# Optimization experiments

Measured on AMD Instinct MI355X. Metric: run time of the kernel, lower is better.

The kernel has to match this reference:

```python
import jax, jax.numpy as jnp
import numpy as np

T, NB, XD, HD, HC = 512, 30, 4096, 512, 32


def gru_cell(x, h, Wih, Whh, bih, bhh):
    # torch nn.GRU gate order: r, z, n
    gi = x @ Wih.T + bih  # [N, 3H]
    gh = h @ Whh.T + bhh
    i_r, i_z, i_n = jnp.split(gi, 3, axis=-1)
    h_r, h_z, h_n = jnp.split(gh, 3, axis=-1)
    r = jax.nn.sigmoid(i_r + h_r)
    z = jax.nn.sigmoid(i_z + h_z)
    n = jnp.tanh(i_n + r * h_n)
    return (1.0 - z) * n + z * h


def setup_inputs() -> dict:
    key = jax.random.key(0)
    ks = jax.random.split(key, 28)
    f32 = jnp.float32
    def rn(k, shape, s=0.05):
        return jax.random.normal(k, shape, dtype=f32) * s
    flow = jax.random.normal(ks[0], (1, T, NB + 1, XD), dtype=f32)
    x = jax.random.normal(ks[1], (1, T, 4), dtype=f32)
    # structured y: track id == bbox slot + 1 when present, 0 otherwise
    present = jax.random.uniform(ks[2], (T, NB)) > 0.3
    present = present.at[:, 0].set(True)
    tid = jnp.where(present, jnp.arange(1, NB + 1)[None, :], 0)
    x1 = jax.random.randint(ks[3], (T, NB), 1, 1080)
    y1 = jax.random.randint(ks[4], (T, NB), 1, 720)
    x2 = jax.random.randint(ks[5], (T, NB), 1, 1080)
    y2 = jax.random.randint(ks[6], (T, NB), 1, 720)
    lab = jax.random.randint(ks[7], (T, NB), 0, 2)
    y = jnp.stack([tid, x1, y1, x2, y2, lab], axis=-1).astype(jnp.int32)[None]
    return {
        'x': x, 'y': y, 'flow': flow,
        'W_phi': rn(ks[8], (XD, HD)), 'b_phi': rn(ks[9], (HD,)),
        'Wih0': rn(ks[10], (3 * HD, 2 * HD)), 'Whh0': rn(ks[11], (3 * HD, HD)),
        'bih0': rn(ks[12], (3 * HD,)), 'bhh0': rn(ks[13], (3 * HD,)),
        'Wih1': rn(ks[14], (3 * HD, HD)), 'Whh1': rn(ks[15], (3 * HD, HD)),
        'bih1': rn(ks[16], (3 * HD,)), 'bhh1': rn(ks[17], (3 * HD,)),
        'Wihc': rn(ks[18], (3 * HC, 4)), 'Whhc': rn(ks[19], (3 * HC, HC)),
        'bihc': rn(ks[20], (3 * HC,)), 'bhhc': rn(ks[21], (3 * HC,)),
        'W1': rn(ks[22], (HD + HC, 256)), 'b1': rn(ks[23], (256,)),
        'W2': rn(ks[24], (256, 2)), 'b2': rn(ks[25], (2,)),
        'wa': rn(ks[26], (HD,)), 'wac': rn(ks[27], (HC,)),
    }


def reference(x, y, flow, W_phi, b_phi, Wih0, Whh0, bih0, bhh0, Wih1, Whh1,
              bih1, bhh1, Wihc, Whhc, bihc, bhhc, W1, b1, W2, b2, wa, wac):
    dt = flow.dtype
    feats = flow[0]      # [T, 31, XD]
    yb_all = y[0]        # [T, 30, 6]
    norm = jnp.array([1080.0, 720.0, 1080.0, 720.0], dtype=dt)

    def att(hmat, w, present):
        # spatial attention: softmax over present tracks of tanh(h) @ w
        s = jnp.tanh(hmat) @ w                               # [30]
        smax = jnp.max(jnp.where(present, s, -1e30))
        e = jnp.where(present, jnp.exp(s - smax), 0.0)
        a = e / jnp.maximum(e.sum(), 1e-9)
        return hmat * a[:, None]

    def step(carry, inp):
        H0, H1, Hc, prev = carry
        feat, yb = inp
        xv = jax.nn.relu(feat @ W_phi + b_phi)               # [31, HD]
        img = jnp.broadcast_to(xv[0], (NB, HD))
        x_t = jnp.concatenate([xv[1:], img], axis=-1)        # [30, 2*HD]
        present = yb[:, 0] != 0
        keep = prev.astype(dt)[:, None]                      # state valid only if track seen last frame
        h0 = H0 * keep
        h1 = H1 * keep
        hc = Hc * keep
        cor = yb[:, 1:5].astype(dt) / norm                   # [30, 4]
        hc_n = gru_cell(cor, hc, Wihc, Whhc, bihc, bhhc)     # [30, HC]
        h0_n = gru_cell(x_t, h0, Wih0, Whh0, bih0, bhh0)     # [30, HD]
        h1_n = gru_cell(h0_n, h1, Wih1, Whh1, bih1, bhh1)    # [30, HD]
        o = jnp.concatenate([h1_n, hc_n], axis=-1)
        o = jax.nn.relu(o @ W1 + b1) @ W2 + b2               # [30, 2]
        logp = jax.nn.log_softmax(o, axis=-1)
        tgt = yb[:, 5].astype(jnp.int32)
        # weighted CE with mean reduction over a single sample == plain NLL
        nll = -jnp.take_along_axis(logp, tgt[:, None], axis=1)[:, 0]
        pm = present.astype(dt)
        loss = jnp.sum(nll * pm)
        H0a = att(h0_n, wa, present)
        H1a = att(h1_n, wa, present)
        Hca = att(hc_n, wac, present)
        return (H0a, H1a, Hca, present), (loss, o * pm[:, None])

    init = (jnp.zeros((NB, HD), dt), jnp.zeros((NB, HD), dt),
            jnp.zeros((NB, HC), dt), jnp.zeros((NB,), bool))
    _, (losses, outs) = jax.lax.scan(step, init, (feats, yb_all))
    return losses.sum(), outs
```

## Files before the change

### kernel.cpp

```cpp
#include <hip/hip_runtime.h>

#define TT   512
#define NBOX 30
#define HDIM 512
#define M1 (TT*31)
#define N1 HDIM
#define K1 4096
#define M2 (TT*NBOX)
#define N2 (3*HDIM)
#define K2 (2*HDIM)
#define NWG 256

#define DYN_FLOATS 40924
#define DYN_BYTES  (DYN_FLOATS * 4)

__device__ __forceinline__ float4 ld4(const float* p) { return *(const float4*)p; }
__device__ __forceinline__ float dot4(float4 a, float4 b) { return a.x*b.x + a.y*b.y + a.z*b.z + a.w*b.w; }
__device__ __forceinline__ float sigf(float x) { return 1.f / (1.f + __expf(-x)); }
__device__ __forceinline__ float thf(float x)  { return 1.f - 2.f / (1.f + __expf(2.f*x)); }

__device__ __forceinline__ float ldg_c(const float* p) {
    return __hip_atomic_load((float*)p, __ATOMIC_RELAXED, __HIP_MEMORY_SCOPE_AGENT);
}
__device__ __forceinline__ void stg_c(float* p, float v) {
    __hip_atomic_store(p, v, __ATOMIC_RELAXED, __HIP_MEMORY_SCOPE_AGENT);
}
__device__ __forceinline__ float2 ldg_c2(const float* p) {
    unsigned long long u = __hip_atomic_load((unsigned long long*)p, __ATOMIC_RELAXED, __HIP_MEMORY_SCOPE_AGENT);
    float2 r;
    r.x = __uint_as_float((unsigned)u);
    r.y = __uint_as_float((unsigned)(u >> 32));
    return r;
}
__device__ __forceinline__ void stg_c2(float* p, float a, float b) {
    unsigned long long u = ((unsigned long long)__float_as_uint(b) << 32) | (unsigned long long)__float_as_uint(a);
    __hip_atomic_store((unsigned long long*)p, u, __ATOMIC_RELAXED, __HIP_MEMORY_SCOPE_AGENT);
}

__global__ __launch_bounds__(256) void gemm_phi(const float* __restrict__ A,
                                                const float* __restrict__ B,
                                                const float* __restrict__ bias,
                                                float* __restrict__ C) {
    __shared__ float As[16][68];
    __shared__ float Bs[16][68];
    const int tid = threadIdx.x;
    const int m0 = blockIdx.x * 64;
    const int n0 = blockIdx.y * 64;
    const int am = tid >> 2, ak = (tid & 3) << 2;
    const int bk = tid >> 4, bn = (tid & 15) << 2;
    const int ty = tid >> 4, tx = tid & 15;
    float acc[4][4] = {};
    for (int k0 = 0; k0 < K1; k0 += 16) {
        const float4 av = *(const float4*)&A[(size_t)(m0 + am) * K1 + k0 + ak];
        const float4 bv = *(const float4*)&B[(size_t)(k0 + bk) * N1 + n0 + bn];
        __syncthreads();
        As[ak + 0][am] = av.x; As[ak + 1][am] = av.y; As[ak + 2][am] = av.z; As[ak + 3][am] = av.w;
        *(float4*)&Bs[bk][bn] = bv;
        __syncthreads();
#pragma unroll
        for (int kk = 0; kk < 16; ++kk) {
            const float4 a = *(const float4*)&As[kk][ty << 2];
            const float4 b = *(const float4*)&Bs[kk][tx << 2];
            const float ar[4] = {a.x, a.y, a.z, a.w};
            const float br[4] = {b.x, b.y, b.z, b.w};
#pragma unroll
            for (int i = 0; i < 4; ++i)
#pragma unroll
                for (int j = 0; j < 4; ++j) acc[i][j] = fmaf(ar[i], br[j], acc[i][j]);
        }
    }
    const float4 bsv = *(const float4*)&bias[n0 + (tx << 2)];
    const float bb[4] = {bsv.x, bsv.y, bsv.z, bsv.w};
#pragma unroll
    for (int i = 0; i < 4; ++i) {
        const int m = m0 + (ty << 2) + i;
        float4 o;
        o.x = fmaxf(acc[i][0] + bb[0], 0.f);
        o.y = fmaxf(acc[i][1] + bb[1], 0.f);
        o.z = fmaxf(acc[i][2] + bb[2], 0.f);
        o.w = fmaxf(acc[i][3] + bb[3], 0.f);
        *(float4*)&C[(size_t)m * N1 + n0 + (tx << 2)] = o;
    }
}

__global__ __launch_bounds__(256) void gemm_gi0(const float* __restrict__ xv,
                                                const float* __restrict__ Wih0,
                                                const float* __restrict__ bih0,
                                                float* __restrict__ C) {
    __shared__ float As[16][68];
    __shared__ float Bs[16][68];
    const int tid = threadIdx.x;
    const int m0 = blockIdx.x * 64;
    const int n0 = blockIdx.y * 64;
    const int am = tid >> 2, ak = (tid & 3) << 2;
    const int bn_ = tid >> 2, bkq = (tid & 3) << 2;
    const int ty = tid >> 4, tx = tid & 15;
    const int r = m0 + am;
    const int t = r / 30;
    const int j = r - t * 30;
    const float* rowTrk = xv + ((size_t)(t * 31 + 1 + j) << 9);
    const float* rowImg = xv + ((size_t)(t * 31) << 9);
    float acc[4][4] = {};
    for (int k0 = 0; k0 < K2; k0 += 16) {
        const int kg = k0 + ak;
        const float4 av = (kg < 512) ? *(const float4*)&rowTrk[kg]
                                     : *(const float4*)&rowImg[kg - 512];
        const float4 wv = *(const float4*)&Wih0[(size_t)(n0 + bn_) * K2 + k0 + bkq];
        __syncthreads();
        As[ak + 0][am] = av.x; As[ak + 1][am] = av.y; As[ak + 2][am] = av.z; As[ak + 3][am] = av.w;
        Bs[bkq + 0][bn_] = wv.x; Bs[bkq + 1][bn_] = wv.y; Bs[bkq + 2][bn_] = wv.z; Bs[bkq + 3][bn_] = wv.w;
        __syncthreads();
#pragma unroll
        for (int kk = 0; kk < 16; ++kk) {
            const float4 a = *(const float4*)&As[kk][ty << 2];
            const float4 b = *(const float4*)&Bs[kk][tx << 2];
            const float ar[4] = {a.x, a.y, a.z, a.w};
            const float br[4] = {b.x, b.y, b.z, b.w};
#pragma unroll
            for (int i = 0; i < 4; ++i)
#pragma unroll
                for (int jq = 0; jq < 4; ++jq) acc[i][jq] = fmaf(ar[i], br[jq], acc[i][jq]);
        }
    }
    const float4 bsv = *(const float4*)&bih0[n0 + (tx << 2)];
    const float bb[4] = {bsv.x, bsv.y, bsv.z, bsv.w};
#pragma unroll
    for (int i = 0; i < 4; ++i) {
        const int m = m0 + (ty << 2) + i;
        float4 o;
        o.x = acc[i][0] + bb[0];
        o.y = acc[i][1] + bb[1];
        o.z = acc[i][2] + bb[2];
        o.w = acc[i][3] + bb[3];
        *(float4*)&C[(size_t)m * N2 + n0 + (tx << 2)] = o;
    }
}

__global__ __launch_bounds__(256) void gic_kernel(const int* __restrict__ y,
                                                  const float* __restrict__ Wihc,
                                                  const float* __restrict__ bihc,
                                                  float* __restrict__ gic) {
    const int idx = blockIdx.x * 256 + threadIdx.x;
    if (idx >= M2 * 96) return;
    const int g = idx % 96;
    const int tj = idx / 96;
    const int* yb = y + (size_t)tj * 6;
    const float c0 = (float)yb[1] * (1.f / 1080.f);
    const float c1 = (float)yb[2] * (1.f / 720.f);
    const float c2 = (float)yb[3] * (1.f / 1080.f);
    const float c3 = (float)yb[4] * (1.f / 720.f);
    gic[idx] = bihc[g] + c0 * Wihc[g * 4 + 0] + c1 * Wihc[g * 4 + 1]
                       + c2 * Wihc[g * 4 + 2] + c3 * Wihc[g * 4 + 3];
}

__global__ void transpose_w1(const float* __restrict__ W1, float* __restrict__ W1T) {
    const int idx = blockIdx.x * 256 + threadIdx.x;
    if (idx >= 544 * 256) return;
    const int c = idx % 544, u = idx / 544;
    W1T[idx] = W1[c * 256 + u];
}

__global__ void init_k(unsigned* bar) {
    for (int i = threadIdx.x; i < 1088; i += 256) bar[i] = 0u;
}

__device__ __forceinline__ void gbar(unsigned* bar, unsigned ep, int w) {
    __syncthreads();
    if (threadIdx.x == 0) {
        asm volatile("" ::: "memory");
        const int g = w >> 4;
        unsigned* gcnt  = bar + g * 32;
        unsigned* gflag = bar + 544 + g * 32;
        const unsigned tgt = ep * 16u;
        unsigned prev = __hip_atomic_fetch_add(gcnt, 1u, __ATOMIC_RELAXED, __HIP_MEMORY_SCOPE_AGENT);
        if (prev + 1u == tgt) {
            unsigned prevr = __hip_atomic_fetch_add(bar + 512, 1u, __ATOMIC_RELAXED, __HIP_MEMORY_SCOPE_AGENT);
            if (prevr + 1u == tgt) {
                for (int i = 0; i < 16; ++i)
                    __hip_atomic_store(bar + 544 + i * 32, ep, __ATOMIC_RELAXED, __HIP_MEMORY_SCOPE_AGENT);
            } else {
                while (__hip_atomic_load(gflag, __ATOMIC_RELAXED, __HIP_MEMORY_SCOPE_AGENT) < ep)
                    __builtin_amdgcn_s_sleep(2);
            }
        } else {
            while (__hip_atomic_load(gflag, __ATOMIC_RELAXED, __HIP_MEMORY_SCOPE_AGENT) < ep)
                __builtin_amdgcn_s_sleep(2);
        }
        asm volatile("" ::: "memory");
    }
    __syncthreads();
}

__device__ __forceinline__ void softmax30_lane(int lane, float sj, int pres, float* outp) {
    float mv = pres ? sj : -1e30f;
    for (int off = 32; off; off >>= 1) mv = fmaxf(mv, __shfl_xor(mv, off));
    float ev = pres ? __expf(sj - mv) : 0.f;
    float sum = ev;
    for (int off = 32; off; off >>= 1) sum += __shfl_xor(sum, off);
    const float inv = 1.f / fmaxf(sum, 1e-9f);
    if (lane < NBOX) outp[lane] = ev * inv;
}

__device__ __forceinline__ void coord_gemv_elem(const float* chc, const float* Whhc, int e, float* cz) {
    const int j = e >> 5, c = e & 31;
    const float* hr = chc + j * 32;
#pragma unroll
    for (int m2 = 0; m2 < 3; ++m2) {
        const float* wr = Whhc + (size_t)(c + 32 * m2) * 32;
        float a = 0.f;
#pragma unroll
        for (int c2 = 0; c2 < 32; c2 += 4) a += dot4(ld4(hr + c2), ld4(wr + c2));
        cz[m2] = a;
    }
}

__device__ __forceinline__ void coord_comb_elem(float* chc, const float* gp, const float* bhhc,
                                                const float* csca, float* hcout, int e, const float* cz) {
    const int j = e >> 5, c = e & 31;
    const float s = csca[j];
    const float r = sigf(gp[j*96 + c]      + s*cz[0] + bhhc[c]);
    const float z = sigf(gp[j*96 + 32 + c] + s*cz[1] + bhhc[32+c]);
    const float n = thf (gp[j*96 + 64 + c] + r*(s*cz[2] + bhhc[64+c]));
    const float hn = (1.f - z)*n + z*(s*chc[e]);
    chc[e] = hn;
    stg_c(hcout + e, hn);
}

struct PArgs {
    const float *gi0, *gic;
    const float *Whh0, *Wih1, *Whh1, *Whhc;
    const float *bhh0, *bih1, *bhh1, *bhhc;
    const float *W1T, *b1, *W2, *b2, *wa, *wac;
    const int *y;
    float *h0g, *h1g, *hcg, *partials, *lossbuf, *out;
    unsigned *bar;
};

__global__ __launch_bounds__(256, 1) void persist(PArgs A) {
    extern __shared__ float smem[];
    float* Hs0  = smem;
    float* Hs1  = smem + 15480;
    float* Wp   = smem + 30960;
    float* gi_s = smem + 40248;
    float* Z0s  = smem + 40428;
    float* Z1s  = smem + 40608;
    float* sm0  = smem + 40788;
    float* sm1  = smem + 40820;
    float* redF = smem + 40852;

    const int w = blockIdx.x;
    const int tid = threadIdx.x;
    const bool isCoord = (w == NWG - 1);
    unsigned ep = 0;
    float lossSum = 0.f;

    if (!isCoord) {
#pragma unroll
        for (int i = 0; i < 9; ++i) {
            const int fid = tid + 256 * i;
            const int slot = fid >> 7;
            const int k4 = (fid & 127) << 2;
            const int sl = slot % 6;
            const int col = (sl % 3) * 512 + 2 * w + ((sl >= 3) ? 1 : 0);
            const float* mat = (slot < 6) ? A.Whh0 : (slot < 12) ? A.Wih1 : A.Whh1;
            *(float4*)&Wp[slot * 516 + k4] = ld4(mat + (size_t)col * 512 + k4);
        }
    } else {
        for (int i = tid; i < 1024; i += 256) Wp[i] = 0.f;
    }
    if (tid < 180) Z1s[tid] = 0.f;

    const int cjX = tid >> 1, ciX = tid & 1, cX = 2 * w + ciX;
    float b0r=0,b0z=0,b0n=0,b1r=0,b1z=0,b1n=0;
    if (tid < 60) {
        b0r = A.bhh0[cX]; b0z = A.bhh0[512+cX]; b0n = A.bhh0[1024+cX];
        b1r = A.bhh1[cX]; b1z = A.bhh1[512+cX]; b1n = A.bhh1[1024+cX];
    }
    float biA = 0.f, biB = 0.f;
    {
        const int q = tid & 7;
        if (tid < 240 && q >= 3 && q < 6) {
            const int slA = 2 * (q - 3), slB = slA + 1;
            biA = A.bih1[(slA % 3) * 512 + 2 * w + ((slA >= 3) ? 1 : 0)];
            biB = A.bih1[(slB % 3) * 512 + 2 * w + ((slB >= 3) ? 1 : 0)];
        }
    }
    float clb=0,c20=0,c21=0, clb2=0,c202=0,c212=0;
    if (!isCoord) { clb = A.b1[w]; c20 = A.W2[2*w]; c21 = A.W2[2*w+1]; }
    if (w == 254) { clb2 = A.b1[255]; c202 = A.W2[510]; c212 = A.W2[511]; }

    float cz0[3]={0,0,0}, cz1[3]={0,0,0}, cz2[3]={0,0,0}, cz3[3]={0,0,0};

    if (tid < 60) {
        const float* gp = A.gi0 + cjX * 1536;
        const float r = sigf(gp[cX] + b0r);
        const float z = sigf(gp[512 + cX] + b0z);
        const float n = thf(gp[1024 + cX] + r * b0n);
        stg_c(A.h0g + cjX * 512 + cX, (1.f - z) * n);
    }
    gbar(A.bar, ++ep, w);

    for (int t = 0; t < TT + 3; ++t) {
        if (t <= 511) {
            const float* src = A.h0g + (t & 1) * 15360;
#pragma unroll
            for (int i = 0; i < 30; ++i) {
                const int e = (tid + 256 * i) << 1;
                *(float2*)&Hs0[(e >> 9) * 516 + (e & 511)] = ldg_c2(src + e);
            }
        }
        if (t >= 1 && t <= 512) {
            const float* src = A.h1g + ((t + 2) % 3) * 15360;
#pragma unroll
            for (int i = 0; i < 30; ++i) {
                const int e = (tid + 256 * i) << 1;
                *(float2*)&Hs1[(e >> 9) * 516 + (e & 511)] = ldg_c2(src + e);
            }
        } else if (t == 0) {
#pragma unroll
            for (int i = 0; i < 30; ++i) {
                const int e = (tid + 256 * i) << 1;
                *(float2*)&Hs1[(e >> 9) * 516 + (e & 511)] = make_float2(0.f, 0.f);
            }
        }
        float g_r = 0.f, g_z = 0.f, g_n = 0.f;
        if (tid < 60 && t <= 510) {
            const float* gp = A.gi0 + (size_t)(t + 1) * 46080 + cjX * 1536;
            g_r = gp[cX]; g_z = gp[512 + cX]; g_n = gp[1024 + cX];
        }
        __syncthreads();

        if (tid < 240 && t <= 511) {
            const int j = tid >> 3, seg = tid & 7;
            const float* wap = A.wa + seg * 64;
            {
                const float* hp = &Hs0[j * 516 + seg * 64];
                float a0 = 0.f;
#pragma unroll 8
                for (int i = 0; i < 64; ++i) a0 += thf(hp[i]) * wap[i];
                a0 += __shfl_down(a0, 4, 8); a0 += __shfl_down(a0, 2, 8); a0 += __shfl_down(a0, 1, 8);
                if (seg == 0) redF[j] = a0;
            }
            if (t >= 1) {
                const float* hp = &Hs1[j * 516 + seg * 64];
                float a1 = 0.f;
#pragma unroll 8
                for (int i = 0; i < 64; ++i) a1 += thf(hp[i]) * wap[i];
                a1 += __shfl_down(a1, 4, 8); a1 += __shfl_down(a1, 2, 8); a1 += __shfl_down(a1, 1, 8);
                if (seg == 0) redF[30 + j] = a1;
            }
        }
        __syncthreads();

        {
            const int wv = tid >> 6;
            if (wv == 0) {
                if (t <= 511) {
                    float sj = 0.f; int pres = 0;
                    if (tid < NBOX) { sj = redF[tid]; pres = (A.y[(size_t)t * 180 + tid * 6] != 0); }
                    softmax30_lane(tid, sj, pres, sm0);
                }
            } else if (wv == 1) {
                const int lane = tid - 64;
                if (t >= 1 && t <= 511) {
                    float sj = 0.f; int pres = 0;
                    if (lane < NBOX) { sj = redF[30 + lane]; pres = (A.y[(size_t)(t - 1) * 180 + lane * 6] != 0); }
                    softmax30_lane(lane, sj, pres, sm1);
                } else if (t == 0) {
                    if (lane < NBOX) sm1[lane] = 0.f;
                }
            } else if (wv == 2 && isCoord && t >= 1 && t <= 512) {
                const int lane = tid - 128;
                float* cscr = Wp + 960;
                float* csca = Wp + 992;
                const int u = t - 1;
                if (u == 0) { if (lane < NBOX) csca[lane] = 0.f; }
                else {
                    float sj = 0.f; int pres = 0;
                    if (lane < NBOX) { sj = cscr[lane]; pres = (A.y[(size_t)(u - 1) * 180 + lane * 6] != 0); }
                    softmax30_lane(lane, sj, pres, csca);
                }
            }
        }
        __syncthreads();

        if (t <= 511 && tid < 240) {
            const int j = tid >> 3, q = tid & 7;
            if (q < 6) {
                const float* hrow = &Hs0[j * 516];
                const int saA = (q < 3) ? (2 * q) : (6 + 2 * (q - 3));
                float a0 = 0.f, a1 = 0.f;
                if (!isCoord) {
                    const float* wA = &Wp[saA * 516];
                    const float* wB = &Wp[(saA + 1) * 516];
#pragma unroll 4
                    for (int k = 0; k < 512; k += 4) {
                        const float4 h4 = ld4(hrow + k);
                        a0 += dot4(h4, ld4(wA + k));
                        a1 += dot4(h4, ld4(wB + k));
                    }
                } else {
                    const int slA = saA % 6, slB = slA + 1;
                    const float* mat = (saA < 6) ? A.Whh0 : A.Wih1;
                    const float* wA = mat + (size_t)((slA % 3) * 512 + 2 * w + ((slA >= 3) ? 1 : 0)) * 512;
                    const float* wB = mat + (size_t)((slB % 3) * 512 + 2 * w + ((slB >= 3) ? 1 : 0)) * 512;
#pragma unroll 4
                    for (int k = 0; k < 512; k += 4) {
                        const float4 h4 = ld4(hrow + k);
                        a0 += dot4(h4, ld4(wA + k));
                        a1 += dot4(h4, ld4(wB + k));
                    }
                }
                if (q < 3) { Z0s[j * 6 + 2 * q] = a0; Z0s[j * 6 + 2 * q + 1] = a1; }
                else { const int g = 2 * (q - 3); gi_s[j * 6 + g] = a0 + biA; gi_s[j * 6 + g + 1] = a1 + biB; }
            }
        }
        if (t >= 1 && t <= 511 && tid < 240) {
            const int j = tid >> 3, q = tid & 7;
            if (q < 3) {
                const float* hrow = &Hs1[j * 516];
                float a0 = 0.f, a1 = 0.f;
                if (!isCoord) {
                    const float* wA = &Wp[(12 + 2 * q) * 516];
                    const float* wB = &Wp[(13 + 2 * q) * 516];
#pragma unroll 4
                    for (int k = 0; k < 512; k += 4) {
                        const float4 h4 = ld4(hrow + k);
                        a0 += dot4(h4, ld4(wA + k));
                        a1 += dot4(h4, ld4(wB + k));
                    }
                } else {
                    const int slA = 2 * q, slB = slA + 1;
                    const float* wA = A.Whh1 + (size_t)((slA % 3) * 512 + 2 * w + ((slA >= 3) ? 1 : 0)) * 512;
                    const float* wB = A.Whh1 + (size_t)((slB % 3) * 512 + 2 * w + ((slB >= 3) ? 1 : 0)) * 512;
#pragma unroll 4
                    for (int k = 0; k < 512; k += 4) {
                        const float4 h4 = ld4(hrow + k);
                        a0 += dot4(h4, ld4(wA + k));
                        a1 += dot4(h4, ld4(wB + k));
                    }
                }
                Z1s[j * 6 + 2 * q] = a0; Z1s[j * 6 + 2 * q + 1] = a1;
            }
        }
        if (isCoord && t >= 1 && t <= 512) {
            const int u = t - 1;
            float* chc = Wp;
            float* csca = Wp + 992;
            const float* gp = A.gic + (size_t)u * 2880;
            float* hcout = A.hcg + (u & 1) * 960;
            if (tid < 960)       coord_comb_elem(chc, gp, A.bhhc, csca, hcout, tid, cz0);
            if (tid + 256 < 960) coord_comb_elem(chc, gp, A.bhhc, csca, hcout, tid + 256, cz1);
            if (tid + 512 < 960) coord_comb_elem(chc, gp, A.bhhc, csca, hcout, tid + 512, cz2);
            if (tid + 768 < 960) coord_comb_elem(chc, gp, A.bhhc, csca, hcout, tid + 768, cz3);
        }
        __syncthreads();

        if (tid < 60 && t <= 511) {
            const float s = sm1[cjX];
            const float r = sigf(gi_s[cjX*6 + ciX*3 + 0] + s * Z1s[cjX*6 + ciX*3 + 0] + b1r);
            const float z = sigf(gi_s[cjX*6 + ciX*3 + 1] + s * Z1s[cjX*6 + ciX*3 + 1] + b1z);
            const float n = thf (gi_s[cjX*6 + ciX*3 + 2] + r * (s * Z1s[cjX*6 + ciX*3 + 2] + b1n));
            const float h1p = Hs1[cjX * 516 + cX];
            stg_c(A.h1g + (t % 3) * 15360 + cjX * 512 + cX, (1.f - z) * n + z * (s * h1p));
        }
        if (tid < 60 && t <= 510) {
            const float s = sm0[cjX];
            const float r = sigf(g_r + s * Z0s[cjX*6 + ciX*3 + 0] + b0r);
            const float z = sigf(g_z + s * Z0s[cjX*6 + ciX*3 + 1] + b0z);
            const float n = thf (g_n + r * (s * Z0s[cjX*6 + ciX*3 + 2] + b0n));
            const float h0p = Hs0[cjX * 516 + cX];
            stg_c(A.h0g + ((t + 1) & 1) * 15360 + cjX * 512 + cX, (1.f - z) * n + z * (s * h0p));
        }
        if (isCoord && t >= 1 && t <= 512) {
            float* chc = Wp;
            float* cscr = Wp + 960;
            if (tid < 960)       coord_gemv_elem(chc, A.Whhc, tid, cz0);
            if (tid + 256 < 960) coord_gemv_elem(chc, A.Whhc, tid + 256, cz1);
            if (tid + 512 < 960) coord_gemv_elem(chc, A.Whhc, tid + 512, cz2);
            if (tid + 768 < 960) coord_gemv_elem(chc, A.Whhc, tid + 768, cz3);
            if (tid < 240) {
                const int j = tid >> 3, seg = tid & 7;
                float p = 0.f;
#pragma unroll
                for (int c2 = seg * 4; c2 < seg * 4 + 4; ++c2) p += thf(chc[j * 32 + c2]) * A.wac[c2];
                p += __shfl_down(p, 4, 8); p += __shfl_down(p, 2, 8); p += __shfl_down(p, 1, 8);
                if (seg == 0) cscr[j] = p;
            }
        }
        if (!isCoord && t >= 2 && t <= 513 && tid < 240) {
            const int v = t - 2;
            const float* h1v = A.h1g + (v % 3) * 15360;
            const float* hcv = A.hcg + (v & 1) * 960;
            const int j = tid >> 3, seg = tid & 7;
            {
                const float* w1r = A.W1T + (size_t)w * 544 + seg * 64;
                const float* hp = h1v + j * 512 + seg * 64;
                float acc = 0.f;
#pragma unroll
                for (int i = 0; i < 32; ++i) {
                    const float2 hv = ldg_c2(hp + 2 * i);
                    acc += hv.x * w1r[2 * i] + hv.y * w1r[2 * i + 1];
                }
                if (seg == 7) {
                    const float* w1h = A.W1T + (size_t)w * 544 + 512;
#pragma unroll
                    for (int i = 0; i < 16; ++i) {
                        const float2 hv = ldg_c2(hcv + j * 32 + 2 * i);
                        acc += hv.x * w1h[2 * i] + hv.y * w1h[2 * i + 1];
                    }
                }
                acc += __shfl_down(acc, 4, 8); acc += __shfl_down(acc, 2, 8); acc += __shfl_down(acc, 1, 8);
                if (seg == 0) {
                    const float uu = fmaxf(clb + acc, 0.f);
                    stg_c2(A.partials + (t & 1) * 16384 + w * 64 + j * 2, uu * c20, uu * c21);
                }
            }
            if (w == 254) {
                const float* w1r = A.W1T + (size_t)255 * 544 + seg * 64;
                const float* hp = h1v + j * 512 + seg * 64;
                float acc = 0.f;
#pragma unroll
                for (int i = 0; i < 32; ++i) {
                    const float2 hv = ldg_c2(hp + 2 * i);
                    acc += hv.x * w1r[2 * i] + hv.y * w1r[2 * i + 1];
                }
                if (seg == 7) {
                    const float* w1h = A.W1T + (size_t)255 * 544 + 512;
#pragma unroll
                    for (int i = 0; i < 16; ++i) {
                        const float2 hv = ldg_c2(hcv + j * 32 + 2 * i);
                        acc += hv.x * w1h[2 * i] + hv.y * w1h[2 * i + 1];
                    }
                }
                acc += __shfl_down(acc, 4, 8); acc += __shfl_down(acc, 2, 8); acc += __shfl_down(acc, 1, 8);
                if (seg == 0) {
                    const float uu = fmaxf(clb2 + acc, 0.f);
                    stg_c2(A.partials + (t & 1) * 16384 + 255 * 64 + j * 2, uu * c202, uu * c212);
                }
            }
        }
        if (w < 30 && t >= 3) {
            const float* pp = A.partials + ((t - 1) & 1) * 16384;
            const float2 v2 = ldg_c2(pp + tid * 64 + w * 2);
            float q0 = v2.x, q1 = v2.y;
            for (int off = 32; off; off >>= 1) { q0 += __shfl_down(q0, off); q1 += __shfl_down(q1, off); }
            if ((tid & 63) == 0) { redF[60 + (tid >> 6) * 2] = q0; redF[61 + (tid >> 6) * 2] = q1; }
        }
        __syncthreads();
        if (w < 30 && t >= 3 && tid == 0) {
            const int f = t - 3;
            float o0 = A.b2[0] + redF[60] + redF[62] + redF[64] + redF[66];
            float o1 = A.b2[1] + redF[61] + redF[63] + redF[65] + redF[67];
            const int* yb = A.y + (size_t)f * 180 + w * 6;
            const float pm = (yb[0] != 0) ? 1.f : 0.f;
            const float m = fmaxf(o0, o1);
            const float lse = m + __logf(__expf(o0 - m) + __expf(o1 - m));
            const float lt = (yb[5] == 0) ? o0 : o1;
            lossSum += pm * (lse - lt);
            A.out[1 + (size_t)f * 60 + w * 2]     = o0 * pm;
            A.out[1 + (size_t)f * 60 + w * 2 + 1] = o1 * pm;
        }
        gbar(A.bar, ++ep, w);
    }

    if (w < 30 && tid == 0) stg_c(A.lossbuf + w, lossSum);
    gbar(A.bar, ++ep, w);
    if (w == 0 && tid == 0) {
        float s = 0.f;
        for (int j = 0; j < NBOX; ++j) s += ldg_c(A.lossbuf + j);
        A.out[0] = s;
    }
}

extern "C" void kernel_launch(void* const* d_in, const int* in_sizes, int n_in,
                              void* d_out, int out_size, void* d_ws, size_t ws_size,
                              hipStream_t stream) {
    (void)in_sizes; (void)n_in; (void)out_size; (void)ws_size;
    const int*   y     = (const int*)d_in[1];
    const float* flow  = (const float*)d_in[2];
    const float* W_phi = (const float*)d_in[3];
    const float* b_phi = (const float*)d_in[4];
    const float* Wih0  = (const float*)d_in[5];
    const float* Whh0  = (const float*)d_in[6];
    const float* bih0  = (const float*)d_in[7];
    const float* bhh0  = (const float*)d_in[8];
    const float* Wih1  = (const float*)d_in[9];
    const float* Whh1  = (const float*)d_in[10];
    const float* bih1  = (const float*)d_in[11];
    const float* bhh1  = (const float*)d_in[12];
    const float* Wihc  = (const float*)d_in[13];
    const float* Whhc  = (const float*)d_in[14];
    const float* bihc  = (const float*)d_in[15];
    const float* bhhc  = (const float*)d_in[16];
    const float* W1    = (const float*)d_in[17];
    const float* b1    = (const float*)d_in[18];
    const float* W2    = (const float*)d_in[19];
    const float* b2    = (const float*)d_in[20];
    const float* wa    = (const float*)d_in[21];
    const float* wac   = (const float*)d_in[22];
    float* out = (float*)d_out;

    float* ws = (float*)d_ws;
    float* xv   = ws;  ws += (size_t)M1 * N1;
    float* gi0  = ws;  ws += (size_t)M2 * N2;
    float* gic  = ws;  ws += (size_t)M2 * 96;
    float* W1T  = ws;  ws += 544 * 256;
    float* h0g  = ws;  ws += 2 * NBOX * 512;
    float* h1g  = ws;  ws += 3 * NBOX * 512;
    float* hcg  = ws;  ws += 2 * NBOX * 32;
    float* partials = ws; ws += 2 * 256 * 64;
    float* lossbuf  = ws; ws += 32;
    unsigned* barmem = (unsigned*)ws; ws += 1088;

    (void)hipFuncSetAttribute((const void*)persist,
                              hipFuncAttributeMaxDynamicSharedMemorySize, DYN_BYTES);

    hipLaunchKernelGGL(init_k, dim3(1), dim3(256), 0, stream, barmem);
    hipLaunchKernelGGL(gemm_phi, dim3(M1 / 64, N1 / 64), dim3(256), 0, stream, flow, W_phi, b_phi, xv);
    hipLaunchKernelGGL(gemm_gi0, dim3(M2 / 64, N2 / 64), dim3(256), 0, stream, xv, Wih0, bih0, gi0);
    hipLaunchKernelGGL(gic_kernel, dim3((M2 * 96 + 255) / 256), dim3(256), 0, stream, y, Wihc, bihc, gic);
    hipLaunchKernelGGL(transpose_w1, dim3((544 * 256 + 255) / 256), dim3(256), 0, stream, W1, W1T);

    PArgs A;
    A.gi0 = gi0; A.gic = gic;
    A.Whh0 = Whh0; A.Wih1 = Wih1; A.Whh1 = Whh1; A.Whhc = Whhc;
    A.bhh0 = bhh0; A.bih1 = bih1; A.bhh1 = bhh1; A.bhhc = bhhc;
    A.W1T = W1T; A.b1 = b1; A.W2 = W2; A.b2 = b2; A.wa = wa; A.wac = wac;
    A.y = y;
    A.h0g = h0g; A.h1g = h1g; A.hcg = hcg;
    A.partials = partials; A.lossbuf = lossbuf; A.out = out;
    A.bar = barmem;
    hipLaunchKernelGGL(persist, dim3(NWG), dim3(256), DYN_BYTES, stream, A);
}
```

Baseline: 36.80 ms.

## Fuse attention scoring into state loads and shorten recurrence pipeline by one step

Attention tanh-dot scores are now computed while h0/h1 are copied into shared memory, using wave shuffles. This removes a separate pass over shared memory and one block barrier per step. The coordinate GRU and the output MLP are shifted one step earlier, with the MLP reading h1 and hc from shared memory, so the scan runs one fewer global-barrier iteration. Whhh1 is no longer staged in LDS and is read from global/cache instead, which shrinks LDS but adds global traffic in the layer-1 GEMV. The barrier spin sleep is also shortened.

```diff
diff --git a/kernel.cpp b/kernel.cpp
--- a/kernel.cpp
+++ b/kernel.cpp
@@ -11,7 +11,7 @@
 #define K2 (2*HDIM)
 #define NWG 256
 
-#define DYN_FLOATS 40924
+#define DYN_FLOATS 38788
 #define DYN_BYTES  (DYN_FLOATS * 4)
 
 __device__ __forceinline__ float4 ld4(const float* p) { return *(const float4*)p; }
@@ -180,11 +180,11 @@
                     __hip_atomic_store(bar + 544 + i * 32, ep, __ATOMIC_RELAXED, __HIP_MEMORY_SCOPE_AGENT);
             } else {
                 while (__hip_atomic_load(gflag, __ATOMIC_RELAXED, __HIP_MEMORY_SCOPE_AGENT) < ep)
-                    __builtin_amdgcn_s_sleep(2);
+                    __builtin_amdgcn_s_sleep(1);
             }
         } else {
             while (__hip_atomic_load(gflag, __ATOMIC_RELAXED, __HIP_MEMORY_SCOPE_AGENT) < ep)
-                __builtin_amdgcn_s_sleep(2);
+                __builtin_amdgcn_s_sleep(1);
         }
         asm volatile("" ::: "memory");
     }
@@ -241,12 +241,15 @@
     float* Hs0  = smem;
     float* Hs1  = smem + 15480;
     float* Wp   = smem + 30960;
-    float* gi_s = smem + 40248;
-    float* Z0s  = smem + 40428;
-    float* Z1s  = smem + 40608;
-    float* sm0  = smem + 40788;
-    float* sm1  = smem + 40820;
-    float* redF = smem + 40852;
+    float* gi_s = smem + 37152;
+    float* Z0s  = smem + 37332;
+    float* Z1s  = smem + 37512;
+    float* sm0  = smem + 37692;
+    float* sm1  = smem + 37724;
+    float* redF = smem + 37756;
+    float* hcs  = smem + 37828;
+    float* s0W = Z0s;
+    float* s1W = Z1s;
 
     const int w = blockIdx.x;
     const int tid = threadIdx.x;
@@ -256,13 +259,13 @@
 
     if (!isCoord) {
 #pragma unroll
-        for (int i = 0; i < 9; ++i) {
+        for (int i = 0; i < 6; ++i) {
             const int fid = tid + 256 * i;
             const int slot = fid >> 7;
             const int k4 = (fid & 127) << 2;
             const int sl = slot % 6;
             const int col = (sl % 3) * 512 + 2 * w + ((sl >= 3) ? 1 : 0);
-            const float* mat = (slot < 6) ? A.Whh0 : (slot < 12) ? A.Wih1 : A.Whh1;
+            const float* mat = (slot < 6) ? A.Whh0 : A.Wih1;
             *(float4*)&Wp[slot * 516 + k4] = ld4(mat + (size_t)col * 512 + k4);
         }
     } else {
@@ -288,6 +291,7 @@
     float clb=0,c20=0,c21=0, clb2=0,c202=0,c212=0;
     if (!isCoord) { clb = A.b1[w]; c20 = A.W2[2*w]; c21 = A.W2[2*w+1]; }
     if (w == 254) { clb2 = A.b1[255]; c202 = A.W2[510]; c212 = A.W2[511]; }
+    const float waX = A.wa[2 * tid], waY = A.wa[2 * tid + 1];
 
     float cz0[3]={0,0,0}, cz1[3]={0,0,0}, cz2[3]={0,0,0}, cz3[3]={0,0,0};
 
@@ -300,55 +304,51 @@
     }
     gbar(A.bar, ++ep, w);
 
-    for (int t = 0; t < TT + 3; ++t) {
+    for (int t = 0; t < TT + 2; ++t) {
         if (t <= 511) {
-            const float* src = A.h0g + (t & 1) * 15360;
+            const float* src = A.h0g + (t & 1) * 15360 + 2 * tid;
 #pragma unroll
             for (int i = 0; i < 30; ++i) {
-                const int e = (tid + 256 * i) << 1;
-                *(float2*)&Hs0[(e >> 9) * 516 + (e & 511)] = ldg_c2(src + e);
-            }
-        }
-        if (t >= 1 && t <= 512) {
-            const float* src = A.h1g + ((t + 2) % 3) * 15360;
+                const float2 v = ldg_c2(src + i * 512);
+                *(float2*)&Hs0[i * 516 + 2 * tid] = v;
+                float p = thf(v.x) * waX + thf(v.y) * waY;
+                p += __shfl_down(p, 32); p += __shfl_down(p, 16); p += __shfl_down(p, 8);
+                p += __shfl_down(p, 4);  p += __shfl_down(p, 2);  p += __shfl_down(p, 1);
+                if ((tid & 63) == 0) s0W[i * 4 + (tid >> 6)] = p;
+            }
+        }
+        if (t == 0) {
+            const float2 zz = make_float2(0.f, 0.f);
+#pragma unroll
+            for (int i = 0; i < 30; ++i) *(float2*)&Hs1[i * 516 + 2 * tid] = zz;
+        } else if (t <= 511) {
+            const float* src = A.h1g + ((t + 2) % 3) * 15360 + 2 * tid;
 #pragma unroll
             for (int i = 0; i < 30; ++i) {
-                const int e = (tid + 256 * i) << 1;
-                *(float2*)&Hs1[(e >> 9) * 516 + (e & 511)] = ldg_c2(src + e);
-            }
-        } else if (t == 0) {
+                const float2 v = ldg_c2(src + i * 512);
+                *(float2*)&Hs1[i * 516 + 2 * tid] = v;
+                float p = thf(v.x) * waX + thf(v.y) * waY;
+                p += __shfl_down(p, 32); p += __shfl_down(p, 16); p += __shfl_down(p, 8);
+                p += __shfl_down(p, 4);  p += __shfl_down(p, 2);  p += __shfl_down(p, 1);
+                if ((tid & 63) == 0) s1W[i * 4 + (tid >> 6)] = p;
+            }
+        } else if (t == 512) {
+            const float* src = A.h1g + ((t + 2) % 3) * 15360 + 2 * tid;
 #pragma unroll
             for (int i = 0; i < 30; ++i) {
-                const int e = (tid + 256 * i) << 1;
-                *(float2*)&Hs1[(e >> 9) * 516 + (e & 511)] = make_float2(0.f, 0.f);
-            }
+                const float2 v = ldg_c2(src + i * 512);
+                *(float2*)&Hs1[i * 516 + 2 * tid] = v;
+            }
+        }
+        if (!isCoord && t >= 1 && t <= 512) {
+            const float* hsrc = A.hcg + ((t - 1) & 1) * 960;
+            for (int fi = tid; fi < 480; fi += 256)
+                *(float2*)&hcs[fi << 1] = ldg_c2(hsrc + (fi << 1));
         }
         float g_r = 0.f, g_z = 0.f, g_n = 0.f;
         if (tid < 60 && t <= 510) {
             const float* gp = A.gi0 + (size_t)(t + 1) * 46080 + cjX * 1536;
             g_r = gp[cX]; g_z = gp[512 + cX]; g_n = gp[1024 + cX];
-        }
-        __syncthreads();
-
-        if (tid < 240 && t <= 511) {
-            const int j = tid >> 3, seg = tid & 7;
-            const float* wap = A.wa + seg * 64;
-            {
-                const float* hp = &Hs0[j * 516 + seg * 64];
-                float a0 = 0.f;
-#pragma unroll 8
-                for (int i = 0; i < 64; ++i) a0 += thf(hp[i]) * wap[i];
-                a0 += __shfl_down(a0, 4, 8); a0 += __shfl_down(a0, 2, 8); a0 += __shfl_down(a0, 1, 8);
-                if (seg == 0) redF[j] = a0;
-            }
-            if (t >= 1) {
-                const float* hp = &Hs1[j * 516 + seg * 64];
-                float a1 = 0.f;
-#pragma unroll 8
-                for (int i = 0; i < 64; ++i) a1 += thf(hp[i]) * wap[i];
-                a1 += __shfl_down(a1, 4, 8); a1 += __shfl_down(a1, 2, 8); a1 += __shfl_down(a1, 1, 8);
-                if (seg == 0) redF[30 + j] = a1;
-            }
         }
         __syncthreads();
 
@@ -357,27 +357,34 @@
             if (wv == 0) {
                 if (t <= 511) {
                     float sj = 0.f; int pres = 0;
-                    if (tid < NBOX) { sj = redF[tid]; pres = (A.y[(size_t)t * 180 + tid * 6] != 0); }
+                    if (tid < NBOX) {
+                        const float4 s4 = ld4(&s0W[tid * 4]);
+                        sj = s4.x + s4.y + s4.z + s4.w;
+                        pres = (A.y[(size_t)t * 180 + tid * 6] != 0);
+                    }
                     softmax30_lane(tid, sj, pres, sm0);
                 }
             } else if (wv == 1) {
                 const int lane = tid - 64;
                 if (t >= 1 && t <= 511) {
                     float sj = 0.f; int pres = 0;
-                    if (lane < NBOX) { sj = redF[30 + lane]; pres = (A.y[(size_t)(t - 1) * 180 + lane * 6] != 0); }
+                    if (lane < NBOX) {
+                        const float4 s4 = ld4(&s1W[lane * 4]);
+                        sj = s4.x + s4.y + s4.z + s4.w;
+                        pres = (A.y[(size_t)(t - 1) * 180 + lane * 6] != 0);
+                    }
                     softmax30_lane(lane, sj, pres, sm1);
                 } else if (t == 0) {
                     if (lane < NBOX) sm1[lane] = 0.f;
                 }
-            } else if (wv == 2 && isCoord && t >= 1 && t <= 512) {
+            } else if (wv == 2 && isCoord && t <= 511) {
                 const int lane = tid - 128;
                 float* cscr = Wp + 960;
                 float* csca = Wp + 992;
-                const int u = t - 1;
-                if (u == 0) { if (lane < NBOX) csca[lane] = 0.f; }
+                if (t == 0) { if (lane < NBOX) csca[lane] = 0.f; }
                 else {
                     float sj = 0.f; int pres = 0;
-                    if (lane < NBOX) { sj = cscr[lane]; pres = (A.y[(size_t)(u - 1) * 180 + lane * 6] != 0); }
+                    if (lane < NBOX) { sj = cscr[lane]; pres = (A.y[(size_t)(t - 1) * 180 + lane * 6] != 0); }
                     softmax30_lane(lane, sj, pres, csca);
                 }
             }
@@ -419,36 +426,24 @@
             const int j = tid >> 3, q = tid & 7;
             if (q < 3) {
                 const float* hrow = &Hs1[j * 516];
+                const int slA = 2 * q, slB = slA + 1;
+                const float* wA = A.Whh1 + (size_t)((slA % 3) * 512 + 2 * w + ((slA >= 3) ? 1 : 0)) * 512;
+                const float* wB = A.Whh1 + (size_t)((slB % 3) * 512 + 2 * w + ((slB >= 3) ? 1 : 0)) * 512;
                 float a0 = 0.f, a1 = 0.f;
-                if (!isCoord) {
-                    const float* wA = &Wp[(12 + 2 * q) * 516];
-                    const float* wB = &Wp[(13 + 2 * q) * 516];
 #pragma unroll 4
-                    for (int k = 0; k < 512; k += 4) {
-                        const float4 h4 = ld4(hrow + k);
-                        a0 += dot4(h4, ld4(wA + k));
-                        a1 += dot4(h4, ld4(wB + k));
-                    }
-                } else {
-                    const int slA = 2 * q, slB = slA + 1;
-                    const float* wA = A.Whh1 + (size_t)((slA % 3) * 512 + 2 * w + ((slA >= 3) ? 1 : 0)) * 512;
-                    const float* wB = A.Whh1 + (size_t)((slB % 3) * 512 + 2 * w + ((slB >= 3) ? 1 : 0)) * 512;
-#pragma unroll 4
-                    for (int k = 0; k < 512; k += 4) {
-                        const float4 h4 = ld4(hrow + k);
-                        a0 += dot4(h4, ld4(wA + k));
-                        a1 += dot4(h4, ld4(wB + k));
-                    }
+                for (int k = 0; k < 512; k += 4) {
+                    const float4 h4 = ld4(hrow + k);
+                    a0 += dot4(h4, ld4(wA + k));
+                    a1 += dot4(h4, ld4(wB + k));
                 }
                 Z1s[j * 6 + 2 * q] = a0; Z1s[j * 6 + 2 * q + 1] = a1;
             }
         }
-        if (isCoord && t >= 1 && t <= 512) {
-            const int u = t - 1;
+        if (isCoord && t <= 511) {
             float* chc = Wp;
             float* csca = Wp + 992;
-            const float* gp = A.gic + (size_t)u * 2880;
-            float* hcout = A.hcg + (u & 1) * 960;
+            const float* gp = A.gic + (size_t)t * 2880;
+            float* hcout = A.hcg + (t & 1) * 960;
             if (tid < 960)       coord_comb_elem(chc, gp, A.bhhc, csca, hcout, tid, cz0);
             if (tid + 256 < 960) coord_comb_elem(chc, gp, A.bhhc, csca, hcout, tid + 256, cz1);
             if (tid + 512 < 960) coord_comb_elem(chc, gp, A.bhhc, csca, hcout, tid + 512, cz2);
@@ -472,7 +467,7 @@
             const float h0p = Hs0[cjX * 516 + cX];
             stg_c(A.h0g + ((t + 1) & 1) * 15360 + cjX * 512 + cX, (1.f - z) * n + z * (s * h0p));
         }
-        if (isCoord && t >= 1 && t <= 512) {
+        if (isCoord && t <= 511) {
             float* chc = Wp;
             float* cscr = Wp + 960;
             if (tid < 960)       coord_gemv_elem(chc, A.Whhc, tid, cz0);
@@ -488,59 +483,51 @@
                 if (seg == 0) cscr[j] = p;
             }
         }
-        if (!isCoord && t >= 2 && t <= 513 && tid < 240) {
-            const int v = t - 2;
-            const float* h1v = A.h1g + (v % 3) * 15360;
-            const float* hcv = A.hcg + (v & 1) * 960;
-            const int j = tid >> 3, seg = tid & 7;
+        if (!isCoord && t >= 1 && t <= 512 && tid < 240) {
+            const int j = tid >> 3, q = tid & 7;
+            const float* hrow = &Hs1[j * 516];
             {
-                const float* w1r = A.W1T + (size_t)w * 544 + seg * 64;
-                const float* hp = h1v + j * 512 + seg * 64;
+                const float* w1r = A.W1T + (size_t)w * 544;
                 float acc = 0.f;
 #pragma unroll
-                for (int i = 0; i < 32; ++i) {
-                    const float2 hv = ldg_c2(hp + 2 * i);
-                    acc += hv.x * w1r[2 * i] + hv.y * w1r[2 * i + 1];
-                }
-                if (seg == 7) {
-                    const float* w1h = A.W1T + (size_t)w * 544 + 512;
-#pragma unroll
-                    for (int i = 0; i < 16; ++i) {
-                        const float2 hv = ldg_c2(hcv + j * 32 + 2 * i);
-                        acc += hv.x * w1h[2 * i] + hv.y * w1h[2 * i + 1];
-                    }
+                for (int i = 0; i < 16; ++i) {
+                    const int k = q * 4 + 32 * i;
+                    acc += dot4(ld4(hrow + k), ld4(w1r + k));
+                }
+                if (q == 7) {
+                    const float* hcr = &hcs[j * 32];
+                    const float* w1h = w1r + 512;
+#pragma unroll
+                    for (int c2 = 0; c2 < 32; c2 += 4) acc += dot4(ld4(hcr + c2), ld4(w1h + c2));
                 }
                 acc += __shfl_down(acc, 4, 8); acc += __shfl_down(acc, 2, 8); acc += __shfl_down(acc, 1, 8);
-                if (seg == 0) {
+                if (q == 0) {
                     const float uu = fmaxf(clb + acc, 0.f);
                     stg_c2(A.partials + (t & 1) * 16384 + w * 64 + j * 2, uu * c20, uu * c21);
                 }
             }
             if (w == 254) {
-                const float* w1r = A.W1T + (size_t)255 * 544 + seg * 64;
-                const float* hp = h1v + j * 512 + seg * 64;
+                const float* w1r = A.W1T + (size_t)255 * 544;
                 float acc = 0.f;
 #pragma unroll
-                for (int i = 0; i < 32; ++i) {
-                    const float2 hv = ldg_c2(hp + 2 * i);
-                    acc += hv.x * w1r[2 * i] + hv.y * w1r[2 * i + 1];
-                }
-                if (seg == 7) {
-                    const float* w1h = A.W1T + (size_t)255 * 544 + 512;
-#pragma unroll
-                    for (int i = 0; i < 16; ++i) {
-                        const float2 hv = ldg_c2(hcv + j * 32 + 2 * i);
-                        acc += hv.x * w1h[2 * i] + hv.y * w1h[2 * i + 1];
-                    }
+                for (int i = 0; i < 16; ++i) {
+                    const int k = q * 4 + 32 * i;
+                    acc += dot4(ld4(hrow + k), ld4(w1r + k));
+                }
+                if (q == 7) {
+                    const float* hcr = &hcs[j * 32];
+                    const float* w1h = w1r + 512;
+#pragma unroll
+                    for (int c2 = 0; c2 < 32; c2 += 4) acc += dot4(ld4(hcr + c2), ld4(w1h + c2));
                 }
                 acc += __shfl_down(acc, 4, 8); acc += __shfl_down(acc, 2, 8); acc += __shfl_down(acc, 1, 8);
-                if (seg == 0) {
+                if (q == 0) {
                     const float uu = fmaxf(clb2 + acc, 0.f);
                     stg_c2(A.partials + (t & 1) * 16384 + 255 * 64 + j * 2, uu * c202, uu * c212);
                 }
             }
         }
-        if (w < 30 && t >= 3) {
+        if (w < 30 && t >= 2) {
             const float* pp = A.partials + ((t - 1) & 1) * 16384;
             const float2 v2 = ldg_c2(pp + tid * 64 + w * 2);
             float q0 = v2.x, q1 = v2.y;
@@ -548,8 +535,8 @@
             if ((tid & 63) == 0) { redF[60 + (tid >> 6) * 2] = q0; redF[61 + (tid >> 6) * 2] = q1; }
         }
         __syncthreads();
-        if (w < 30 && t >= 3 && tid == 0) {
-            const int f = t - 3;
+        if (w < 30 && t >= 2 && tid == 0) {
+            const int f = t - 2;
             float o0 = A.b2[0] + redF[60] + redF[62] + redF[64] + redF[66];
             float o1 = A.b2[1] + redF[61] + redF[63] + redF[65] + redF[67];
             const int* yb = A.y + (size_t)f * 180 + w * 6;
```

Measured after the change: 43.95 ms. 1.19x slower.
